# Kernel tuning notes

Hardware: AMD Instinct MI355X
Metric: run time of the kernel (lower is better)

## Reference

```python
import jax, jax.numpy as jnp
import numpy as np

_R, _C = 64, 64
_N = _R * _C
_SEC_PER_A = 31556926.0
_K = 0.01        # sheet_conductivity
_ALPHA = 1.25    # sheet_flow_exp
_HR = 0.1        # bedrock_step_height
_LR = 2.0        # cavity_spacing
_A = 5e-25       # cavity_closure_coeff
_NEXP = 3        # Glen exponent


def _build_grid():
    idx = np.arange(_N).reshape(_R, _C)
    tail = np.concatenate([idx[:, :-1].ravel(), idx[:-1, :].ravel()]).astype(np.int32)
    head = np.concatenate([idx[:, 1:].ravel(), idx[1:, :].ravel()]).astype(np.int32)
    L = tail.size
    links_at_node = -np.ones((_N, 4), np.int32)
    adj = -np.ones((_N, 4), np.int32)
    cnt = np.zeros(_N, np.int32)
    for l in range(L):
        for a, b in ((tail[l], head[l]), (head[l], tail[l])):
            links_at_node[a, cnt[a]] = l
            adj[a, cnt[a]] = b
            cnt[a] += 1
    r, c = np.divmod(np.arange(_N), _C)
    status = ((r == 0) | (r == _R - 1) | (c == 0) | (c == _C - 1)).astype(np.int32)
    return tail, head, links_at_node, adj, status


def setup_inputs():
    key = jax.random.key(0)
    k = jax.random.split(key, 8)
    tail, head, links_at_node, adj, status = _build_grid()
    L = tail.size
    bedrock = jax.random.uniform(k[0], (_N,), jnp.float32, 0.0, 500.0)
    ice_thk = jax.random.uniform(k[1], (_N,), jnp.float32, 100.0, 1000.0)
    overburden = 917.0 * 9.81 * ice_thk
    base_potential = 1000.0 * 9.81 * bedrock + overburden
    potential = base_potential - 0.3 * overburden + 1e3 * jax.random.normal(k[2], (_N,), jnp.float32)
    sheet_thickness = jax.random.uniform(k[3], (_N,), jnp.float32, 0.01, 0.1)
    sliding_velocity = jax.random.uniform(k[4], (L,), jnp.float32, 10.0, 100.0)
    specific_melt_rate = jax.random.uniform(k[5], (_N,), jnp.float32, 1e-7, 1e-6)
    link_length = jnp.full((L,), 100.0, jnp.float32)
    adj_j = jnp.asarray(adj)
    # mean over ALL 4 slots, padded entries contribute 0 (matches original jnp.mean)
    adj_pot = jnp.mean(jnp.where(adj_j != -1, base_potential[adj_j], 0.0), axis=1)
    inflow = jnp.where(base_potential > adj_pot, 1, -1) * (jnp.asarray(status) > 0)
    return dict(
        base_potential=base_potential,
        overburden_pressure=overburden,
        specific_melt_rate=specific_melt_rate,
        sheet_thickness=sheet_thickness,
        potential=potential,
        sliding_velocity=sliding_velocity,
        link_length=link_length,
        link_tail=jnp.asarray(tail),
        link_head=jnp.asarray(head),
        links_at_node=jnp.asarray(links_at_node),
        inflow_outflow=inflow.astype(jnp.int32),
        dt=3600,
    )


def reference(base_potential, overburden_pressure, specific_melt_rate, sheet_thickness,
              potential, sliding_velocity, link_length, link_tail, link_head,
              links_at_node, inflow_outflow, dt):
    N = base_potential.shape[0]
    t, h = link_tail, link_head
    # --- elliptic operator assembly (per-link, scatter into dense [N,N]) ---
    sheets = 0.5 * (sheet_thickness[t] + sheet_thickness[h])
    inv_grad = jnp.abs((potential[t] - potential[h]) / link_length) ** (-0.5)
    c = -_K * sheets ** _ALPHA * link_length * inv_grad  # symmetric link coefficient (<0)
    dir_row = inflow_outflow == 1  # Dirichlet rows
    ct = jnp.where(dir_row[t], 0.0, c)  # contribution into row tail
    ch = jnp.where(dir_row[h], 0.0, c)  # contribution into row head
    M = (jnp.zeros((N, N), base_potential.dtype)
         .at[t, h].add(ct).at[h, t].add(ch)
         .at[t, t].add(-ct).at[h, h].add(-ch))
    M = jnp.where(dir_row[:, None], jnp.eye(N, dtype=M.dtype), M)
    forcing = jnp.where(dir_row, base_potential - overburden_pressure, specific_melt_rate)
    new_potential = jnp.linalg.solve(M, forcing)
    # --- sheet thickness: map_mean_of_links_to_node then Newton on node-local ODE ---
    valid = links_at_node != -1
    lv = (sliding_velocity / _SEC_PER_A)[links_at_node]  # [N,4]
    sliding = jnp.abs(jnp.sum(jnp.where(valid, lv, 0.0), axis=1)
                      / jnp.maximum(valid.sum(axis=1), 1))
    pressure = base_potential - new_potential
    dtf = jnp.asarray(dt, base_potential.dtype)
    # residual r(h) = h - h0 - dt*(sliding*(HR-h)/LR - A*P^n*h) is LINEAR in h,
    # so Newton converges in one exact step -> closed form:
    new_h = (sheet_thickness + dtf * sliding * _HR / _LR) / (
        1.0 + dtf * (sliding / _LR + _A * pressure ** _NEXP))
    return new_potential, new_h
```

## Files before the change

### kernel.cpp

```cpp
#include <hip/hip_runtime.h>
#include <math.h>


#define NT    512
#define NPT   8
#define NN    4096
#define NC    1024
#define NCC   256
#define CCIT  20
#define MAXIT 40

enum : int { RSHL1 = 0x101, RSHR1 = 0x111,
             ROR8 = 0x128, ROR12 = 0x12C, ROR14 = 0x12E, ROR15 = 0x12F,
             WSHL1 = 0x130, WSHR1 = 0x138 };

__device__ __forceinline__ void barL() {
    asm volatile("s_waitcnt lgkmcnt(0)" ::: "memory");
    __builtin_amdgcn_s_barrier();
    asm volatile("" ::: "memory");
}

template<int CTRL>
__device__ __forceinline__ float dppf(float x) {
    return __int_as_float(__builtin_amdgcn_update_dpp(
        __float_as_int(x), __float_as_int(x), CTRL, 0xF, 0xF, false));
}
template<int CTRL>
__device__ __forceinline__ double dppd(double x) {
    const int lo = __double2loint(x), hi = __double2hiint(x);
    const int l2 = __builtin_amdgcn_update_dpp(lo, lo, CTRL, 0xF, 0xF, false);
    const int h2 = __builtin_amdgcn_update_dpp(hi, hi, CTRL, 0xF, 0xF, false);
    return __hiloint2double(h2, l2);
}
__device__ __forceinline__ void pl16sw(int& a, int& b) {
    asm volatile("s_nop 1\n\tv_permlane16_swap_b32 %0, %1" : "+v"(a), "+v"(b));
}
__device__ __forceinline__ void pl32sw(int& a, int& b) {
    asm volatile("s_nop 1\n\tv_permlane32_swap_b32 %0, %1" : "+v"(a), "+v"(b));
}
__device__ __forceinline__ float shift_dn16(float x, bool inR2) {
    int a = __float_as_int(x), b = __float_as_int(x);
    pl16sw(a, b);
    int g = b, g2 = b;
    pl32sw(g, g2);
    return __int_as_float(inR2 ? g : a);
}
__device__ __forceinline__ float shift_up16(float x, bool inR1) {
    int a = __float_as_int(x), b = __float_as_int(x);
    pl16sw(a, b);
    int d1 = __float_as_int(x), d2 = __float_as_int(x);
    pl32sw(d1, d2);
    int e1 = d2, e2 = d2;
    pl16sw(e1, e2);
    return __int_as_float(inR1 ? e1 : b);
}
__device__ __forceinline__ double dsw32(double x) {
    int lo = __double2loint(x), hi = __double2hiint(x);
    int a = lo, b = lo; pl32sw(a, b);
    int c = hi, d = hi; pl32sw(c, d);
    return __hiloint2double(d, b);
}
__device__ __forceinline__ double dsw16(double x) {
    int lo = __double2loint(x), hi = __double2hiint(x);
    int a = lo, b = lo; pl16sw(a, b);
    int c = hi, d = hi; pl16sw(c, d);
    return __hiloint2double(d, b);
}

__global__ __launch_bounds__(NT, 2)
void sds_solver(const float* __restrict__ base_pot,
                const float* __restrict__ ovb,
                const float* __restrict__ melt,
                const float* __restrict__ sheet,
                const float* __restrict__ pot,
                const float* __restrict__ svel,
                const float* __restrict__ llen,
                const int*   __restrict__ ltail,
                const int*   __restrict__ lhead,
                const int*   __restrict__ lan,
                const int*   __restrict__ inflow,
                const int*   __restrict__ dt_raw,
                float* __restrict__ out,
                int N, int L)
{
    __shared__ __align__(16) float cW[NN], cE[NN], cN[NN], cS[NN];
    __shared__ __align__(16) float FD[NN];
    __shared__ __align__(16) float BNDA[8*128], BNDB[8*128];
    __shared__ __align__(16) float CB[32 + NC + 32];
    __shared__ __align__(16) float CB2[32 + NC + 32];
    __shared__ __align__(16) float EB[32 + NC + 32];
    __shared__ __align__(16) float IDC[32 + NC + 32];
    __shared__ __align__(16) float ccb[NCC];
    __shared__ __align__(16) float cWc_s[NC], cEc_s[NC], cNc_s[NC], cSc_s[NC], dc_s[NC];
    __shared__ double redp[32], redg[16];

    const int tid  = threadIdx.x;
    const int lane = tid & 63;
    const int wid  = tid >> 6;
    const int nb0  = (wid << 9) + lane;

    if (N != NN || L != 8064) return;

    const int dti = dt_raw[0];
    const float as_f = __int_as_float(dti);
    const double dtf = (as_f > 0.5f && as_f < 1.0e12f) ? (double)as_f : (double)dti;

    const float invthf = 0.8f;
    const float c1f = 0.2195122f, c2f = 0.9756098f;
    const float wA = 1.75f;

    {
        const float4 z4 = make_float4(0.f, 0.f, 0.f, 0.f);
        #pragma unroll
        for (int i = tid; i < NN/4; i += NT) {
            ((float4*)cW)[i] = z4; ((float4*)cE)[i] = z4;
            ((float4*)cN)[i] = z4; ((float4*)cS)[i] = z4;
        }
        if (tid < 32) {
            CB[tid]=0.f;  CB[32+NC+tid]=0.f;
            CB2[tid]=0.f; CB2[32+NC+tid]=0.f;
            EB[tid]=0.f;  EB[32+NC+tid]=0.f;
            IDC[tid]=0.f; IDC[32+NC+tid]=0.f;
        }
    }
    __syncthreads();

    for (int l = tid; l < 8064; l += NT) {
        int t, h;
        if (l < 4032) {
            const int r = l / 63;
            const int c2 = l - r * 63;
            t = (r << 6) + c2; h = t + 1;
        } else {
            t = l - 4032; h = t + 64;
        }
        const float sheets = 0.5f * (sheet[t] + sheet[h]);
        const float len = llen[l];
        const float grad = fabsf((pot[t] - pot[h]) / len);
        const float c = -0.01f * (sheets * sqrtf(sqrtf(sheets))) * len / sqrtf(grad);
        const bool dt_ = (inflow[t] == 1);
        const bool dh_ = (inflow[h] == 1);
        if (l < 4032) { cE[t] = dt_ ? 0.f : c; cW[h] = dh_ ? 0.f : c; }
        else          { cS[t] = dt_ ? 0.f : c; cN[h] = dh_ ? 0.f : c; }
    }
    __syncthreads();

    float cw[NPT], ce[NPT], cn[NPT], cs[NPT], dgf[NPT], invdf[NPT];
    float xv[NPT], rv[NPT];
    bool dirf[NPT];
    auto ldco = [&]() {
        #pragma unroll
        for (int k = 0; k < NPT; ++k) {
            const int n = nb0 + (k << 6);
            cw[k] = cW[n]; ce[k] = cE[n]; cn[k] = cN[n]; cs[k] = cS[n];
        }
    };
    ldco();
    double gsum = 0.0, gcnt = 0.0;
    #pragma unroll
    for (int k = 0; k < NPT; ++k) {
        const int n = nb0 + (k << 6);
        const bool dir = (inflow[n] == 1);
        const double d = -((double)cw[k] + (double)ce[k] + (double)cn[k] + (double)cs[k]);
        const double dg = (dir || d == 0.0) ? 1.0 : d;
        dgf[k] = (float)dg; invdf[k] = (float)(1.0 / dg);
        dirf[k] = dir;
        if (dir) {
            const double g = (double)base_pot[n] - (double)ovb[n];
            gsum += g; gcnt += 1.0;
        }
    }
    {
        #pragma unroll
        for (int off = 32; off > 0; off >>= 1) {
            gsum += __shfl_down(gsum, off, 64);
            gcnt += __shfl_down(gcnt, off, 64);
        }
        if (lane == 0) { redg[2*wid] = gsum; redg[2*wid+1] = gcnt; }
        __syncthreads();
        gsum = 0.0; gcnt = 0.0;
        #pragma unroll
        for (int w = 0; w < NT/64; ++w) { gsum += redg[2*w]; gcnt += redg[2*w+1]; }
    }
    const double gmean = gsum / (gcnt > 0.0 ? gcnt : 1.0);

    auto stB = [&](float* B, const float* v) {
        *(float2*)&B[(wid << 7) + (lane << 1)] = make_float2(v[0], v[7]);
    };
    float qf[NPT];
    auto spmvC = [&](const float* B, const float* vr) {
        const float nb = B[(((wid + 7) & 7) << 7) + (lane << 1) + 1];
        const float sb = B[(((wid + 1) & 7) << 7) + (lane << 1) + 0];
        #pragma unroll
        for (int k = 0; k < NPT; ++k) {
            const float wv = dppf<WSHR1>(vr[k]);
            const float ev = dppf<WSHL1>(vr[k]);
            const float nv = k ? vr[k-1] : nb;
            const float sv = (k < NPT-1) ? vr[k+1] : sb;
            qf[k] = dgf[k]*vr[k] + cw[k]*wv + ce[k]*ev + cn[k]*nv + cs[k]*sv;
        }
    };

    {
        float x0r[NPT];
        #pragma unroll
        for (int k = 0; k < NPT; ++k) {
            const int n = nb0 + (k << 6);
            const double g = (double)base_pot[n] - (double)ovb[n];
            const float x0f = (float)(dirf[k] ? g : gmean);
            xv[k] = x0f; x0r[k] = x0f;
        }
        stB(BNDA, x0r); __syncthreads();
        spmvC(BNDA, x0r);
        #pragma unroll
        for (int k = 0; k < NPT; ++k) {
            const int n = nb0 + (k << 6);
            rv[k] = dirf[k] ? 0.f
                  : (float)((double)melt[n] - (double)qf[k]);
        }
    }
    __syncthreads();

    {
        #pragma unroll
        for (int k = 0; k < NPT; ++k) {
            const int n = nb0 + (k << 6);
            if (lane != 0  && inflow[n-1]  == 1) cW[n] = 0.f;
            if (lane != 63 && inflow[n+1]  == 1) cE[n] = 0.f;
            if (n >= 64        && inflow[n-64] == 1) cN[n] = 0.f;
            if (n < NN-64      && inflow[n+64] == 1) cS[n] = 0.f;
            FD[n] = dirf[k] ? 0.f : dgf[k];
        }
    }
    __syncthreads();
    ldco();

    #pragma unroll
    for (int q = 0; q < 2; ++q) {
        const int I = 2*tid + q;
        const int R = tid >> 4, C = I & 31;
        const int na = 128*R + 2*C, nbq = na+1, nc_ = na+64, nd = na+65;
        cEc_s[I] = cE[nbq] + cE[nd];
        cWc_s[I] = cW[na] + cW[nc_];
        cNc_s[I] = cN[na] + cN[nbq];
        cSc_s[I] = cS[nc_] + cS[nd];
        const float d = FD[na]+FD[nbq]+FD[nc_]+FD[nd]
                      + 2.0f*(cE[na] + cE[nc_] + cS[na] + cS[nbq]);
        dc_s[I] = (d > 0.f) ? d : 1.0f;
    }
    __syncthreads();

    float cwc[2], cec[2], cnc[2], csc[2], dcr[2], invdc[2];
    {
        float2 t;
        t = *(float2*)&cWc_s[2*tid]; cwc[0]=t.x; cwc[1]=t.y;
        t = *(float2*)&cEc_s[2*tid]; cec[0]=t.x; cec[1]=t.y;
        t = *(float2*)&cNc_s[2*tid]; cnc[0]=t.x; cnc[1]=t.y;
        t = *(float2*)&cSc_s[2*tid]; csc[0]=t.x; csc[1]=t.y;
        t = *(float2*)&dc_s[2*tid];  dcr[0]=t.x; dcr[1]=t.y;
        invdc[0] = 1.0f/dcr[0]; invdc[1] = 1.0f/dcr[1];
        *(float2*)&IDC[32 + 2*tid] = make_float2(invdc[0], invdc[1]);
    }
    float cwcc[4], cecc[4], cncc[4], cscc[4], dccr[4], invdcc[4];
    if (tid < 64) {
        #pragma unroll
        for (int j = 0; j < 4; ++j) {
            const int Rc = ((tid >> 4) << 2) + j, Cc = tid & 15;
            const int IA = 64*Rc + 2*Cc, IB = IA+1, IC = IA+32, ID = IA+33;
            cecc[j] = cEc_s[IB] + cEc_s[ID];
            cwcc[j] = cWc_s[IA] + cWc_s[IC];
            cncc[j] = cNc_s[IA] + cNc_s[IB];
            cscc[j] = cSc_s[IC] + cSc_s[ID];
            const float d = dc_s[IA]+dc_s[IB]+dc_s[IC]+dc_s[ID]
                          + 2.0f*(cEc_s[IA] + cEc_s[IC] + cSc_s[IA] + cSc_s[IB]);
            dccr[j] = (d > 0.f) ? d : 1.0f;
            invdcc[j] = 1.0f/dccr[j];
        }
    }
    float c1cc[CCIT+1], c2cc[CCIT+1], invthcc;
    {
        const double a = 8e-3, b2 = 2.0;
        const double th = 0.5*(b2+a), de = 0.5*(b2-a), s1 = th/de;
        double rp = 1.0/s1;
        for (int j = 1; j <= CCIT; ++j) {
            const double rj = 1.0/(2.0*s1 - rp);
            c1cc[j] = (float)(rj*rp);
            c2cc[j] = (float)(2.0*rj/de);
            rp = rj;
        }
        invthcc = (float)(1.0/th);
    }
    auto cspmv = [&](const float* B_, float v0, float v1, float& q0, float& q1) {
        const float2 up = *(const float2*)&B_[2*tid];
        const float2 dn = *(const float2*)&B_[64 + 2*tid];
        const float wv = dppf<WSHR1>(v1);
        const float ev = dppf<WSHL1>(v0);
        q0 = dcr[0]*v0 + cwc[0]*wv + cec[0]*v1 + cnc[0]*up.x + csc[0]*dn.x;
        q1 = dcr[1]*v1 + cwc[1]*v0 + cec[1]*ev + cnc[1]*up.y + csc[1]*dn.y;
    };

    double rho_prev = 0.0, pap = 0.0, tol = 0.0;
    float pv[NPT], sv[NPT], rpv[NPT];
    #pragma unroll
    for (int k = 0; k < NPT; ++k) { pv[k]=0.f; sv[k]=0.f; rpv[k]=0.f; }

    for (int it = 0; it < MAXIT; ++it) {
        float f0[NPT], d0[NPT], d1[NPT], zpre[NPT];
        #pragma unroll
        for (int k = 0; k < NPT; ++k) { f0[k] = rv[k] * invdf[k]; d0[k] = f0[k] * invthf; }
        stB(BNDA, d0); barL();
        spmvC(BNDA, d0);
        #pragma unroll
        for (int k = 0; k < NPT; ++k) {
            const float f1 = f0[k] - qf[k]*invdf[k];
            d1[k] = c1f*d0[k] + c2f*f1;
            zpre[k] = d0[k] + d1[k];
            f0[k] = f1;
        }
        stB(BNDB, d1); barL();
        spmvC(BNDB, d1);

        float r1[NPT], t2[NPT];
        #pragma unroll
        for (int k = 0; k < NPT; ++k) {
            const float fres = f0[k] - qf[k]*invdf[k];
            r1[k] = dirf[k] ? 0.f : dgf[k]*fres;
        }
        #pragma unroll
        for (int k = 0; k < NPT; ++k) t2[k] = r1[k] + dppf<WSHL1>(r1[k]);
        if ((lane & 1) == 0) {
            #pragma unroll
            for (int j = 0; j < 4; ++j)
                CB2[32 + ((wid << 2) + j)*32 + (lane >> 1)] = t2[2*j] + t2[2*j+1];
        }
        barL();

        float rc[2], f0c[2], d0c[2], d1c[2], qc0, qc1;
        {
            const float2 rcl = *(const float2*)&CB2[32 + 2*tid];
            rc[0] = rcl.x; rc[1] = rcl.y;
        }
        #pragma unroll
        for (int q = 0; q < 2; ++q) {
            f0c[q] = rc[q] * invdc[q];
            d0c[q] = f0c[q] * invthf;
        }
        {
            const float2 ru = *(const float2*)&CB2[2*tid];
            const float2 rd = *(const float2*)&CB2[64 + 2*tid];
            const float2 iu = *(const float2*)&IDC[2*tid];
            const float2 id = *(const float2*)&IDC[64 + 2*tid];
            const float wv = dppf<WSHR1>(d0c[1]);
            const float ev = dppf<WSHL1>(d0c[0]);
            qc0 = dcr[0]*d0c[0] + cwc[0]*wv + cec[0]*d0c[1]
                + cnc[0]*((ru.x*iu.x)*invthf) + csc[0]*((rd.x*id.x)*invthf);
            qc1 = dcr[1]*d0c[1] + cwc[1]*d0c[0] + cec[1]*ev
                + cnc[1]*((ru.y*iu.y)*invthf) + csc[1]*((rd.y*id.y)*invthf);
        }
        {
            const float f1a = f0c[0] - qc0*invdc[0];
            const float f1b = f0c[1] - qc1*invdc[1];
            d1c[0] = c1f*d0c[0] + c2f*f1a;
            d1c[1] = c1f*d0c[1] + c2f*f1b;
            f0c[0] = f1a; f0c[1] = f1b;
        }
        *(float2*)&EB[32 + 2*tid] = make_float2(d1c[0], d1c[1]);
        barL();
        cspmv(EB, d1c[0], d1c[1], qc0, qc1);
        {
            const float fra = f0c[0] - qc0*invdc[0];
            const float frb = f0c[1] - qc1*invdc[1];
            *(float2*)&CB[32 + 2*tid] = make_float2(dcr[0]*fra, dcr[1]*frb);
        }
        barL();

        if (tid < 64) {
            const int cc_c  = tid & 15;
            const int cc_rb = tid >> 4;
            const bool inR1 = (cc_rb == 1), inR2 = (cc_rb == 2);
            float fr[4], dr[4], zc[4];
            #pragma unroll
            for (int j = 0; j < 4; ++j) {
                const int IA = (((cc_rb << 2) + j) << 6) + (cc_c << 1);
                const float rcc = CB[32+IA] + CB[32+IA+1] + CB[32+IA+32] + CB[32+IA+33];
                fr[j] = rcc * invdcc[j];
                dr[j] = fr[j] * invthcc;
                zc[j] = dr[j];
            }
            for (int s = 1; s <= CCIT; ++s) {
                const float zN = shift_dn16(dr[3], inR2);
                const float zS = shift_up16(dr[0], inR1);
                float qcc[4];
                #pragma unroll
                for (int j = 0; j < 4; ++j) {
                    const float wj = dppf<RSHR1>(dr[j]);
                    const float ej = dppf<RSHL1>(dr[j]);
                    const float nj = j ? dr[j-1] : zN;
                    const float sj = (j < 3) ? dr[j+1] : zS;
                    qcc[j] = dccr[j]*dr[j] + cwcc[j]*wj + cecc[j]*ej
                           + cncc[j]*nj + cscc[j]*sj;
                }
                #pragma unroll
                for (int j = 0; j < 4; ++j) {
                    fr[j] -= qcc[j] * invdcc[j];
                    dr[j]  = c1cc[s]*dr[j] + c2cc[s]*fr[j];
                    zc[j] += dr[j];
                }
            }
            #pragma unroll
            for (int j = 0; j < 4; ++j)
                ccb[(((cc_rb << 2) + j) << 4) + cc_c] = zc[j];
        }
        barL();

        const float ecv = wA * ccb[16*(tid >> 5) + (tid & 15)];
        float zmc[2] = { d0c[0] + d1c[0] + ecv, d0c[1] + d1c[1] + ecv };
        {
            const float2 ru = *(const float2*)&CB2[2*tid];
            const float2 rd = *(const float2*)&CB2[64 + 2*tid];
            const float2 iu = *(const float2*)&IDC[2*tid];
            const float2 id = *(const float2*)&IDC[64 + 2*tid];
            const float2 du = *(const float2*)&EB[2*tid];
            const float2 dd = *(const float2*)&EB[64 + 2*tid];
            const int R = tid >> 4;
            const int Ru = (R > 0)  ? R - 1 : 0;
            const int Rd = (R < 31) ? R + 1 : 31;
            const float ecu = wA * ccb[(Ru >> 1)*16 + (tid & 15)];
            const float ecd = wA * ccb[(Rd >> 1)*16 + (tid & 15)];
            const float upx = ((ru.x*iu.x)*invthf + du.x) + ecu;
            const float upy = ((ru.y*iu.y)*invthf + du.y) + ecu;
            const float dnx = ((rd.x*id.x)*invthf + dd.x) + ecd;
            const float dny = ((rd.y*id.y)*invthf + dd.y) + ecd;
            const float wv = dppf<WSHR1>(zmc[1]);
            const float ev = dppf<WSHL1>(zmc[0]);
            qc0 = dcr[0]*zmc[0] + cwc[0]*wv + cec[0]*zmc[1] + cnc[0]*upx + csc[0]*dnx;
            qc1 = dcr[1]*zmc[1] + cwc[1]*zmc[0] + cec[1]*ev + cnc[1]*upy + csc[1]*dny;
        }
        float fmc[2] = { (rc[0]-qc0)*invdc[0], (rc[1]-qc1)*invdc[1] };
        float d0p[2] = { fmc[0]*invthf, fmc[1]*invthf };
        *(float2*)&CB[32 + 2*tid] = make_float2(d0p[0], d0p[1]);
        barL();
        cspmv(CB, d0p[0], d0p[1], qc0, qc1);
        {
            const float f1a = fmc[0] - qc0*invdc[0];
            const float f1b = fmc[1] - qc1*invdc[1];
            const float efa = zmc[0] + c1f*d0p[0] + c2f*f1a + d0p[0];
            const float efb = zmc[1] + c1f*d0p[1] + c2f*f1b + d0p[1];
            *(float2*)&EB[32 + 2*tid] = make_float2(efa, efb);
        }
        barL();

        float ec[4];
        #pragma unroll
        for (int j = 0; j < 4; ++j)
            ec[j] = EB[32 + ((wid << 2) + j)*32 + (lane >> 1)];
        float zmid[NPT], zf[NPT];
        #pragma unroll
        for (int k = 0; k < NPT; ++k)
            zmid[k] = zpre[k] + (dirf[k] ? 0.f : wA * ec[k >> 1]);
        stB(BNDA, zmid); barL();
        spmvC(BNDA, zmid);
        float fmid[NPT], d0q[NPT];
        #pragma unroll
        for (int k = 0; k < NPT; ++k) {
            fmid[k] = rv[k]*invdf[k] - qf[k]*invdf[k];
            d0q[k]  = fmid[k] * invthf;
        }
        stB(BNDB, d0q); barL();
        spmvC(BNDB, d0q);
        #pragma unroll
        for (int k = 0; k < NPT; ++k) {
            const float f1 = fmid[k] - qf[k]*invdf[k];
            zf[k] = zmid[k] + d0q[k] + c1f*d0q[k] + c2f*f1;
        }
        stB(BNDA, zf); barL();
        spmvC(BNDA, zf);

        double rho_n = 0.0, rzp = 0.0, zw = 0.0, pw = 0.0;
        #pragma unroll
        for (int k = 0; k < NPT; ++k) {
            const double zk = (double)zf[k], wk = (double)qf[k];
            rho_n += (double)rv[k]  * zk;
            rzp   += (double)rpv[k] * zk;
            zw    += zk * wk;
            pw    += (double)pv[k] * wk;
        }
        rho_n += dsw32(rho_n); rzp += dsw32(rzp); zw += dsw32(zw); pw += dsw32(pw);
        rho_n += dsw16(rho_n); rzp += dsw16(rzp); zw += dsw16(zw); pw += dsw16(pw);
        rho_n += dppd<ROR8 >(rho_n); rzp += dppd<ROR8 >(rzp); zw += dppd<ROR8 >(zw); pw += dppd<ROR8 >(pw);
        rho_n += dppd<ROR12>(rho_n); rzp += dppd<ROR12>(rzp); zw += dppd<ROR12>(zw); pw += dppd<ROR12>(pw);
        rho_n += dppd<ROR14>(rho_n); rzp += dppd<ROR14>(rzp); zw += dppd<ROR14>(zw); pw += dppd<ROR14>(pw);
        rho_n += dppd<ROR15>(rho_n); rzp += dppd<ROR15>(rzp); zw += dppd<ROR15>(zw); pw += dppd<ROR15>(pw);
        if (lane == 0) {
            redp[4*wid] = rho_n; redp[4*wid+1] = rzp;
            redp[4*wid+2] = zw;  redp[4*wid+3] = pw;
        }
        barL();
        rho_n = 0.0; rzp = 0.0; zw = 0.0; pw = 0.0;
        #pragma unroll
        for (int w = 0; w < NT/64; ++w) {
            rho_n += redp[4*w];   rzp += redp[4*w+1];
            zw    += redp[4*w+2]; pw  += redp[4*w+3];
        }

        if (it == 0) {
            tol = rho_n * 1e-3 + 1e-300;
            if (!(rho_n > 0.0)) break;
        } else if (rho_n <= tol || !(rho_n > 0.0)) break;
        const double beta = (it == 0) ? 0.0
                          : fmax(0.0, (rho_n - rzp) / rho_prev);
        pap = zw + beta * (2.0 * pw + beta * pap);
        if (!(pap > 0.0)) break;
        const double alpha = rho_n / pap;
        rho_prev = rho_n;
        const float alpha_f = (float)alpha, beta_f = (float)beta;
        #pragma unroll
        for (int k = 0; k < NPT; ++k) {
            rpv[k] = rv[k];
            pv[k] = zf[k] + beta_f * pv[k];
            sv[k] = qf[k] + beta_f * sv[k];
            xv[k] += alpha_f * pv[k];
            rv[k] -= alpha_f * sv[k];
        }
    }

    #pragma unroll
    for (int k = 0; k < NPT; ++k) {
        const int n = nb0 + (k << 6);
        const int r = (wid << 3) + k, c2 = lane;
        const double g = (double)base_pot[n] - (double)ovb[n];
        const double x = dirf[k] ? g : (double)xv[k];

        const int hb = r * 63 + c2;
        float sva = 0.0f; int cnt = 0;
        if (c2 > 0)  { sva += svel[hb - 1];       cnt++; }
        if (c2 < 63) { sva += svel[hb];           cnt++; }
        if (r  > 0)  { sva += svel[4032 + n - 64]; cnt++; }
        if (r  < 63) { sva += svel[4032 + n];      cnt++; }
        const double sliding =
            fabs((double)sva / 31556926.0 / (double)(cnt > 0 ? cnt : 1));
        const double P   = (double)base_pot[n] - x;
        const double num = (double)sheet[n] + dtf * sliding * 0.1 / 2.0;
        const double den = 1.0 + dtf * (sliding / 2.0 + 5e-25 * P * P * P);
        out[n]      = (float)x;
        out[NN + n] = (float)(num / den);
    }
}

extern "C" void kernel_launch(void* const* d_in, const int* in_sizes, int n_in,
                              void* d_out, int out_size, void* d_ws, size_t ws_size,
                              hipStream_t stream) {
    const float* base_pot = (const float*)d_in[0];
    const float* ovb      = (const float*)d_in[1];
    const float* melt     = (const float*)d_in[2];
    const float* sheet    = (const float*)d_in[3];
    const float* pot      = (const float*)d_in[4];
    const float* svel     = (const float*)d_in[5];
    const float* llen     = (const float*)d_in[6];
    const int*   ltail    = (const int*)d_in[7];
    const int*   lhead    = (const int*)d_in[8];
    const int*   lan      = (const int*)d_in[9];
    const int*   inflow   = (const int*)d_in[10];
    const int*   dt_raw   = (const int*)d_in[11];
    float* out = (float*)d_out;
    const int N = in_sizes[0];
    const int L = in_sizes[5];

    hipLaunchKernelGGL(sds_solver, dim3(1), dim3(NT), 0, stream,
                       base_pot, ovb, melt, sheet, pot, svel, llen,
                       ltail, lhead, lan, inflow, dt_raw, out, N, L);
}
```

Measured before the change: 131.0 us.

## Replicate halo residuals per warp to drop a barrier from the CG loop

Each warp now tracks the residual and search-direction values of its neighbouring warps' boundary rows (ghost cells), updated from a shared qf boundary buffer written before the existing reduction barrier. This lets the first preconditioner SpMV use register ghosts instead of a store-plus-barrier exchange. It also drops the stored previous-residual array and recomputes r_prev·z as rho + alpha_prev·(s·z), which removes registers. The cost is redundant ghost arithmetic, an extra shared store per iteration, and possible floating-point drift between the replicated ghosts and the owning warp's values.

```diff
diff --git a/kernel.cpp b/kernel.cpp
--- a/kernel.cpp
+++ b/kernel.cpp
@@ -86,6 +86,7 @@
     __shared__ __align__(16) float cW[NN], cE[NN], cN[NN], cS[NN];
     __shared__ __align__(16) float FD[NN];
     __shared__ __align__(16) float BNDA[8*128], BNDB[8*128];
+    __shared__ __align__(16) float QFB[8*128];
     __shared__ __align__(16) float CB[32 + NC + 32];
     __shared__ __align__(16) float CB2[32 + NC + 32];
     __shared__ __align__(16) float EB[32 + NC + 32];
@@ -156,6 +157,21 @@
         }
     };
     ldco();
+    float invdga = 1.0f, invdgb = 1.0f;
+    if (wid > 0) {
+        const int ng = nb0 - 64;
+        const bool dirg = (inflow[ng] == 1);
+        const double d = -((double)cW[ng] + (double)cE[ng] + (double)cN[ng] + (double)cS[ng]);
+        const double dg = (dirg || d == 0.0) ? 1.0 : d;
+        invdga = (float)(1.0 / dg);
+    }
+    if (wid < 7) {
+        const int ng = nb0 + 512;
+        const bool dirg = (inflow[ng] == 1);
+        const double d = -((double)cW[ng] + (double)cE[ng] + (double)cN[ng] + (double)cS[ng]);
+        const double dg = (dirg || d == 0.0) ? 1.0 : d;
+        invdgb = (float)(1.0 / dg);
+    }
     double gsum = 0.0, gcnt = 0.0;
     #pragma unroll
     for (int k = 0; k < NPT; ++k) {
@@ -201,6 +217,7 @@
         }
     };
 
+    float rga = 0.f, rgb = 0.f, sga = 0.f, sgb = 0.f;
     {
         float x0r[NPT];
         #pragma unroll
@@ -218,8 +235,11 @@
             rv[k] = dirf[k] ? 0.f
                   : (float)((double)melt[n] - (double)qf[k]);
         }
+        stB(BNDB, rv);
     }
     __syncthreads();
+    rga = (wid > 0) ? BNDB[((wid - 1) << 7) + (lane << 1) + 1] : 0.f;
+    rgb = (wid < 7) ? BNDB[((wid + 1) << 7) + (lane << 1) + 0] : 0.f;
 
     {
         #pragma unroll
@@ -299,17 +319,27 @@
         q1 = dcr[1]*v1 + cwc[1]*v0 + cec[1]*ev + cnc[1]*up.y + csc[1]*dn.y;
     };
 
-    double rho_prev = 0.0, pap = 0.0, tol = 0.0;
-    float pv[NPT], sv[NPT], rpv[NPT];
+    double rho_prev = 0.0, pap = 0.0, tol = 0.0, alpha_prev = 0.0;
+    float pv[NPT], sv[NPT];
     #pragma unroll
-    for (int k = 0; k < NPT; ++k) { pv[k]=0.f; sv[k]=0.f; rpv[k]=0.f; }
+    for (int k = 0; k < NPT; ++k) { pv[k]=0.f; sv[k]=0.f; }
 
     for (int it = 0; it < MAXIT; ++it) {
         float f0[NPT], d0[NPT], d1[NPT], zpre[NPT];
         #pragma unroll
         for (int k = 0; k < NPT; ++k) { f0[k] = rv[k] * invdf[k]; d0[k] = f0[k] * invthf; }
-        stB(BNDA, d0); barL();
-        spmvC(BNDA, d0);
+        const float f0ga = rga * invdga;
+        const float d0ga = f0ga * invthf;
+        const float f0gb = rgb * invdgb;
+        const float d0gb = f0gb * invthf;
+        #pragma unroll
+        for (int k = 0; k < NPT; ++k) {
+            const float wv = dppf<WSHR1>(d0[k]);
+            const float ev = dppf<WSHL1>(d0[k]);
+            const float nv = k ? d0[k-1] : d0ga;
+            const float sv_ = (k < NPT-1) ? d0[k+1] : d0gb;
+            qf[k] = dgf[k]*d0[k] + cw[k]*wv + ce[k]*ev + cn[k]*nv + cs[k]*sv_;
+        }
         #pragma unroll
         for (int k = 0; k < NPT; ++k) {
             const float f1 = f0[k] - qf[k]*invdf[k];
@@ -476,30 +506,31 @@
         stB(BNDA, zf); barL();
         spmvC(BNDA, zf);
 
-        double rho_n = 0.0, rzp = 0.0, zw = 0.0, pw = 0.0;
+        double rho_n = 0.0, szv = 0.0, zw = 0.0, pw = 0.0;
         #pragma unroll
         for (int k = 0; k < NPT; ++k) {
             const double zk = (double)zf[k], wk = (double)qf[k];
-            rho_n += (double)rv[k]  * zk;
-            rzp   += (double)rpv[k] * zk;
+            rho_n += (double)rv[k] * zk;
+            szv   += (double)sv[k] * zk;
             zw    += zk * wk;
             pw    += (double)pv[k] * wk;
         }
-        rho_n += dsw32(rho_n); rzp += dsw32(rzp); zw += dsw32(zw); pw += dsw32(pw);
-        rho_n += dsw16(rho_n); rzp += dsw16(rzp); zw += dsw16(zw); pw += dsw16(pw);
-        rho_n += dppd<ROR8 >(rho_n); rzp += dppd<ROR8 >(rzp); zw += dppd<ROR8 >(zw); pw += dppd<ROR8 >(pw);
-        rho_n += dppd<ROR12>(rho_n); rzp += dppd<ROR12>(rzp); zw += dppd<ROR12>(zw); pw += dppd<ROR12>(pw);
-        rho_n += dppd<ROR14>(rho_n); rzp += dppd<ROR14>(rzp); zw += dppd<ROR14>(zw); pw += dppd<ROR14>(pw);
-        rho_n += dppd<ROR15>(rho_n); rzp += dppd<ROR15>(rzp); zw += dppd<ROR15>(zw); pw += dppd<ROR15>(pw);
+        rho_n += dsw32(rho_n); szv += dsw32(szv); zw += dsw32(zw); pw += dsw32(pw);
+        rho_n += dsw16(rho_n); szv += dsw16(szv); zw += dsw16(zw); pw += dsw16(pw);
+        rho_n += dppd<ROR8 >(rho_n); szv += dppd<ROR8 >(szv); zw += dppd<ROR8 >(zw); pw += dppd<ROR8 >(pw);
+        rho_n += dppd<ROR12>(rho_n); szv += dppd<ROR12>(szv); zw += dppd<ROR12>(zw); pw += dppd<ROR12>(pw);
+        rho_n += dppd<ROR14>(rho_n); szv += dppd<ROR14>(szv); zw += dppd<ROR14>(zw); pw += dppd<ROR14>(pw);
+        rho_n += dppd<ROR15>(rho_n); szv += dppd<ROR15>(szv); zw += dppd<ROR15>(zw); pw += dppd<ROR15>(pw);
+        *(float2*)&QFB[(wid << 7) + (lane << 1)] = make_float2(qf[0], qf[7]);
         if (lane == 0) {
-            redp[4*wid] = rho_n; redp[4*wid+1] = rzp;
+            redp[4*wid] = rho_n; redp[4*wid+1] = szv;
             redp[4*wid+2] = zw;  redp[4*wid+3] = pw;
         }
         barL();
-        rho_n = 0.0; rzp = 0.0; zw = 0.0; pw = 0.0;
+        rho_n = 0.0; szv = 0.0; zw = 0.0; pw = 0.0;
         #pragma unroll
         for (int w = 0; w < NT/64; ++w) {
-            rho_n += redp[4*w];   rzp += redp[4*w+1];
+            rho_n += redp[4*w];   szv += redp[4*w+1];
             zw    += redp[4*w+2]; pw  += redp[4*w+3];
         }
 
@@ -507,20 +538,29 @@
             tol = rho_n * 1e-3 + 1e-300;
             if (!(rho_n > 0.0)) break;
         } else if (rho_n <= tol || !(rho_n > 0.0)) break;
+        const double rzp = rho_n + alpha_prev * szv;
         const double beta = (it == 0) ? 0.0
                           : fmax(0.0, (rho_n - rzp) / rho_prev);
         pap = zw + beta * (2.0 * pw + beta * pap);
         if (!(pap > 0.0)) break;
         const double alpha = rho_n / pap;
         rho_prev = rho_n;
+        alpha_prev = alpha;
         const float alpha_f = (float)alpha, beta_f = (float)beta;
         #pragma unroll
         for (int k = 0; k < NPT; ++k) {
-            rpv[k] = rv[k];
             pv[k] = zf[k] + beta_f * pv[k];
             sv[k] = qf[k] + beta_f * sv[k];
             xv[k] += alpha_f * pv[k];
             rv[k] -= alpha_f * sv[k];
+        }
+        {
+            const float qga = (wid > 0) ? QFB[((wid - 1) << 7) + (lane << 1) + 1] : 0.f;
+            sga = qga + beta_f * sga;
+            rga -= alpha_f * sga;
+            const float qgb = (wid < 7) ? QFB[((wid + 1) << 7) + (lane << 1) + 0] : 0.f;
+            sgb = qgb + beta_f * sgb;
+            rgb -= alpha_f * sgb;
         }
     }
 
```

Measured after the change: 134.4 us. 1.03x slower.
